# Performance work log

Hardware: AMD Instinct MI355X
Metric: run time of the kernel (lower is better)

## Reference

```python
import jax, jax.numpy as jnp
import numpy as np

# GLOM level-1 geometry (img 256x320, patch 8): feature map 32x40, embd 128
B, C, H, W = 16, 128, 32, 40
GRID = 40          # grid_size = max(256//8, 320//8)
STD = 8.0          # att_stds[0] = int(1/8 * 2**(1+1+4)) with std_scale=4
ATT_TEMP = 1.2     # att_temp_mode 'two', level 1, scale 1.0
EPS = 1e-5


def _norm_cdf(z):
    return 0.5 * (1.0 + jax.scipy.special.erf(z * (1.0 / np.sqrt(2.0))))


def _build_probs():
    # Gaussian-distance neighbor-sampling probabilities, as in GLOM.__init__
    coords = jnp.arange(GRID, dtype=jnp.float32) / STD
    ii, jj = jnp.meshgrid(coords, coords, indexing='ij')          # [G,G]
    pts = jnp.stack([ii.ravel(), jj.ravel()], axis=-1)            # [G*G,2]
    diff = pts[:, None, :] - pts[None, :, :]
    dists = jnp.sqrt(jnp.sum(diff * diff, axis=-1))               # [G*G,G*G]
    p = _norm_cdf(dists + 1.0 / STD) - _norm_cdf(dists)
    p = p * (1.0 - jnp.eye(GRID * GRID, dtype=jnp.float32))       # zero diagonal
    p = jnp.maximum(p, 0.0)
    p = p.reshape(GRID, GRID, GRID, GRID)
    return p[:H, :W, :H, :W]                                      # [H,W,H,W]


def setup_inputs() -> dict:
    key = jax.random.key(0)
    k_x, = jax.random.split(key, 1)
    x = jax.random.normal(k_x, (B, C, H, W), dtype=jnp.float32)
    probs = _build_probs().astype(jnp.float32)
    gamma = jnp.ones((C,), dtype=jnp.float32)
    beta = jnp.zeros((C,), dtype=jnp.float32)
    return {"x": x, "probs": probs, "gamma": gamma, "beta": beta}


def reference(x, probs, gamma, beta):
    # x: [B,C,H,W] level embeddings; probs: [H,W,H,W] distance weights
    b, c, h, w = x.shape
    n = h * w
    xf = x.reshape(b, c, n).transpose(0, 2, 1)                     # [B,N,C]
    # temperature-scaled embedding similarity attention
    logits = jnp.einsum('bnc,bmc->bnm', xf, xf) / (ATT_TEMP * np.sqrt(c))
    att = jax.nn.softmax(logits, axis=-1)                          # [B,N,N]
    # weight by Gaussian-distance neighbor probabilities, renormalize
    wts = att * probs.reshape(n, n)[None]
    wts = wts / (jnp.sum(wts, axis=-1, keepdims=True) + 1e-8)
    agg = jnp.einsum('bnm,bmc->bnc', wts, xf)                      # [B,N,C]
    out = agg.transpose(0, 2, 1).reshape(b, c, h, w)
    # InstanceNorm2d (affine) fused on the attention output
    mu = jnp.mean(out, axis=(2, 3), keepdims=True)
    var = jnp.var(out, axis=(2, 3), keepdims=True)
    out = (out - mu) * jax.lax.rsqrt(var + EPS)
    out = out * gamma[None, :, None, None] + beta[None, :, None, None]
    return out
```

## Files before the change

kernel.cpp:

```cpp
#include <hip/hip_runtime.h>
#include <hip/hip_bf16.h>


#define B_ 16
#define C_ 128
#define N_ 1280
#define BN 80
#define BM 128
#define NT 10
#define LDH 136

typedef __attribute__((ext_vector_type(8))) short short8;
typedef __attribute__((ext_vector_type(4))) float f32x4;
typedef __attribute__((ext_vector_type(4))) unsigned short us4_t;

#define MFMA16(a, bb, c) __builtin_amdgcn_mfma_f32_16x16x32_bf16((a), (bb), (c), 0, 0, 0)

__device__ __forceinline__ unsigned short f2bf(float f) {
    unsigned u = __builtin_bit_cast(unsigned, f);
    u = (u + 0x7FFFu + ((u >> 16) & 1u)) >> 16;
    return (unsigned short)u;
}

__global__ __launch_bounds__(256, 1) void glom_attn_mfma(
    const float* __restrict__ x, const float* __restrict__ probs,
    float* __restrict__ out)
{
    __shared__ __attribute__((aligned(16))) unsigned short AnT[BN][LDH];
    __shared__ __attribute__((aligned(16))) unsigned short XmT[BM][LDH];
    __shared__ __attribute__((aligned(16))) unsigned short Xm [C_][LDH];
    __shared__ __attribute__((aligned(16))) unsigned short Plds[BN][LDH];
    __shared__ float Sred[4][BN], Tred[4][BN], invd_s[BN];

    const int tid = threadIdx.x;
    const int w   = tid >> 6;
    const int l   = tid & 63;
    const int a   = l & 15;
    const int g   = l >> 4;

    const int L  = blockIdx.x;
    const int b  = (L & 7) + 8 * (L >> 7);
    const int nt = (L >> 3) & 15;
    const int n0 = nt * BN;
    const float* Xb = x + (size_t)b * C_ * N_;

    const float INV_SCALE = 0.07365695637359846f;

    #pragma unroll
    for (int k = 0; k < 10; ++k) {
        int f  = tid + 256 * k;
        int c  = f / 20;
        int i4 = f % 20;
        const float4 v = *reinterpret_cast<const float4*>(Xb + c * N_ + n0 + i4 * 4);
        AnT[i4 * 4 + 0][c] = f2bf(v.x);
        AnT[i4 * 4 + 1][c] = f2bf(v.y);
        AnT[i4 * 4 + 2][c] = f2bf(v.z);
        AnT[i4 * 4 + 3][c] = f2bf(v.w);
    }

    f32x4 Y[2][5];
    #pragma unroll
    for (int cl = 0; cl < 2; ++cl)
        #pragma unroll
        for (int nt2 = 0; nt2 < 5; ++nt2)
            #pragma unroll
            for (int rr = 0; rr < 4; ++rr) Y[cl][nt2][rr] = 0.0f;

    float Sp[5][4], Tp[5][4];
    #pragma unroll
    for (int nt2 = 0; nt2 < 5; ++nt2)
        #pragma unroll
        for (int rr = 0; rr < 4; ++rr) { Sp[nt2][rr] = 0.0f; Tp[nt2][rr] = 0.0f; }

    const int cg = tid >> 3, mg = tid & 7;

    for (int mt = 0; mt < NT; ++mt) {
        const int mg0 = mt * BM;
        __syncthreads();

        #pragma unroll
        for (int q = 0; q < 4; ++q) {
            const int mcol = mg0 + 4 * mg + 32 * q;
            const float4 r0 = *reinterpret_cast<const float4*>(Xb + (4*cg+0)*N_ + mcol);
            const float4 r1 = *reinterpret_cast<const float4*>(Xb + (4*cg+1)*N_ + mcol);
            const float4 r2 = *reinterpret_cast<const float4*>(Xb + (4*cg+2)*N_ + mcol);
            const float4 r3 = *reinterpret_cast<const float4*>(Xb + (4*cg+3)*N_ + mcol);
            const int ml = 4 * mg + 32 * q;
            *reinterpret_cast<us4_t*>(&Xm[4*cg+0][ml]) = (us4_t){f2bf(r0.x), f2bf(r0.y), f2bf(r0.z), f2bf(r0.w)};
            *reinterpret_cast<us4_t*>(&Xm[4*cg+1][ml]) = (us4_t){f2bf(r1.x), f2bf(r1.y), f2bf(r1.z), f2bf(r1.w)};
            *reinterpret_cast<us4_t*>(&Xm[4*cg+2][ml]) = (us4_t){f2bf(r2.x), f2bf(r2.y), f2bf(r2.z), f2bf(r2.w)};
            *reinterpret_cast<us4_t*>(&Xm[4*cg+3][ml]) = (us4_t){f2bf(r3.x), f2bf(r3.y), f2bf(r3.z), f2bf(r3.w)};
            *reinterpret_cast<unsigned*>(&XmT[ml+0][4*cg+0]) = (unsigned)f2bf(r0.x) | ((unsigned)f2bf(r1.x) << 16);
            *reinterpret_cast<unsigned*>(&XmT[ml+0][4*cg+2]) = (unsigned)f2bf(r2.x) | ((unsigned)f2bf(r3.x) << 16);
            *reinterpret_cast<unsigned*>(&XmT[ml+1][4*cg+0]) = (unsigned)f2bf(r0.y) | ((unsigned)f2bf(r1.y) << 16);
            *reinterpret_cast<unsigned*>(&XmT[ml+1][4*cg+2]) = (unsigned)f2bf(r2.y) | ((unsigned)f2bf(r3.y) << 16);
            *reinterpret_cast<unsigned*>(&XmT[ml+2][4*cg+0]) = (unsigned)f2bf(r0.z) | ((unsigned)f2bf(r1.z) << 16);
            *reinterpret_cast<unsigned*>(&XmT[ml+2][4*cg+2]) = (unsigned)f2bf(r2.z) | ((unsigned)f2bf(r3.z) << 16);
            *reinterpret_cast<unsigned*>(&XmT[ml+3][4*cg+0]) = (unsigned)f2bf(r0.w) | ((unsigned)f2bf(r1.w) << 16);
            *reinterpret_cast<unsigned*>(&XmT[ml+3][4*cg+2]) = (unsigned)f2bf(r2.w) | ((unsigned)f2bf(r3.w) << 16);
        }
        __syncthreads();

        f32x4 d1[2][5];
        #pragma unroll
        for (int jj = 0; jj < 2; ++jj)
            #pragma unroll
            for (int nt2 = 0; nt2 < 5; ++nt2)
                #pragma unroll
                for (int rr = 0; rr < 4; ++rr) d1[jj][nt2][rr] = 0.0f;

        #pragma unroll
        for (int ks = 0; ks < 4; ++ks) {
            const short8 b0 = *reinterpret_cast<const short8*>(&XmT[32*w      + a][32*ks + 8*g]);
            const short8 b1 = *reinterpret_cast<const short8*>(&XmT[32*w + 16 + a][32*ks + 8*g]);
            #pragma unroll
            for (int nt2 = 0; nt2 < 5; ++nt2) {
                const short8 a1 = *reinterpret_cast<const short8*>(&AnT[16*nt2 + a][32*ks + 8*g]);
                d1[0][nt2] = MFMA16(a1, b0, d1[0][nt2]);
                d1[1][nt2] = MFMA16(a1, b1, d1[1][nt2]);
            }
        }

        #pragma unroll
        for (int jj = 0; jj < 2; ++jj) {
            #pragma unroll
            for (int nt2 = 0; nt2 < 5; ++nt2) {
                const int mcol = mg0 + 32*w + 16*jj + a;
                const size_t pbase = (size_t)(n0 + 16*nt2 + 4*g) * N_ + mcol;
                #pragma unroll
                for (int rr = 0; rr < 4; ++rr) {
                    const float e  = __expf(d1[jj][nt2][rr] * INV_SCALE);
                    const float p  = probs[pbase + (size_t)rr * N_];
                    const float wv = e * p;
                    Sp[nt2][rr] += e;
                    Tp[nt2][rr] += wv;
                    Plds[16*nt2 + 4*g + rr][32*w + 16*jj + a] = f2bf(wv);
                }
            }
        }
        __syncthreads();

        #pragma unroll
        for (int ks2 = 0; ks2 < 4; ++ks2) {
            const short8 a20 = *reinterpret_cast<const short8*>(&Xm[32*w      + a][32*ks2 + 8*g]);
            const short8 a21 = *reinterpret_cast<const short8*>(&Xm[32*w + 16 + a][32*ks2 + 8*g]);
            #pragma unroll
            for (int nt2 = 0; nt2 < 5; ++nt2) {
                const short8 b2 = *reinterpret_cast<const short8*>(&Plds[16*nt2 + a][32*ks2 + 8*g]);
                Y[0][nt2] = MFMA16(a20, b2, Y[0][nt2]);
                Y[1][nt2] = MFMA16(a21, b2, Y[1][nt2]);
            }
        }
    }

    #pragma unroll
    for (int nt2 = 0; nt2 < 5; ++nt2)
        #pragma unroll
        for (int rr = 0; rr < 4; ++rr) {
            #pragma unroll
            for (int d = 1; d < 16; d <<= 1) {
                Sp[nt2][rr] += __shfl_xor(Sp[nt2][rr], d);
                Tp[nt2][rr] += __shfl_xor(Tp[nt2][rr], d);
            }
        }
    if (a == 0) {
        #pragma unroll
        for (int nt2 = 0; nt2 < 5; ++nt2)
            #pragma unroll
            for (int rr = 0; rr < 4; ++rr) {
                Sred[w][16*nt2 + 4*g + rr] = Sp[nt2][rr];
                Tred[w][16*nt2 + 4*g + rr] = Tp[nt2][rr];
            }
    }
    __syncthreads();
    if (tid < BN) {
        const float S = Sred[0][tid] + Sred[1][tid] + Sred[2][tid] + Sred[3][tid];
        const float T = Tred[0][tid] + Tred[1][tid] + Tred[2][tid] + Tred[3][tid];
        invd_s[tid] = 1.0f / (T + 1e-8f * S);
    }
    __syncthreads();

    #pragma unroll
    for (int nt2 = 0; nt2 < 5; ++nt2) {
        const float iv = invd_s[16*nt2 + a];
        #pragma unroll
        for (int cl = 0; cl < 2; ++cl)
            #pragma unroll
            for (int rr = 0; rr < 4; ++rr)
                out[((size_t)b * C_ + 32*w + 16*cl + 4*g + rr) * N_ + n0 + 16*nt2 + a]
                    = Y[cl][nt2][rr] * iv;
    }
}

__global__ __launch_bounds__(256, 4) void glom_inorm_kernel(
    float* __restrict__ out, const float* __restrict__ gamma,
    const float* __restrict__ beta)
{
    const int row = blockIdx.x;
    const int c   = row & (C_ - 1);
    float* p = out + (size_t)row * N_;
    const int t = threadIdx.x;

    float v[5];
    float sm = 0.0f;
    #pragma unroll
    for (int k = 0; k < 5; ++k) { v[k] = p[t + 256 * k]; sm += v[k]; }
    #pragma unroll
    for (int d = 1; d < 64; d <<= 1) sm += __shfl_xor(sm, d);

    __shared__ float red[4];
    const int wid = t >> 6;
    if ((t & 63) == 0) red[wid] = sm;
    __syncthreads();
    const float mu = (red[0] + red[1] + red[2] + red[3]) * (1.0f / (float)N_);

    float sq = 0.0f;
    #pragma unroll
    for (int k = 0; k < 5; ++k) { float d0 = v[k] - mu; sq += d0 * d0; }
    #pragma unroll
    for (int d = 1; d < 64; d <<= 1) sq += __shfl_xor(sq, d);
    __syncthreads();
    if ((t & 63) == 0) red[wid] = sq;
    __syncthreads();
    const float var = (red[0] + red[1] + red[2] + red[3]) * (1.0f / (float)N_);
    const float rs  = rsqrtf(var + 1e-5f);
    const float g   = gamma[c];
    const float be  = beta[c];
    #pragma unroll
    for (int k = 0; k < 5; ++k)
        p[t + 256 * k] = (v[k] - mu) * rs * g + be;
}

extern "C" void kernel_launch(void* const* d_in, const int* in_sizes, int n_in,
                              void* d_out, int out_size, void* d_ws, size_t ws_size,
                              hipStream_t stream)
{
    (void)in_sizes; (void)n_in; (void)out_size; (void)d_ws; (void)ws_size;
    const float* x     = (const float*)d_in[0];
    const float* probs = (const float*)d_in[1];
    const float* gamma = (const float*)d_in[2];
    const float* beta  = (const float*)d_in[3];
    float* out = (float*)d_out;

    glom_attn_mfma<<<dim3(256), dim3(256), 0, stream>>>(x, probs, out);
    glom_inorm_kernel<<<dim3(B_ * C_), dim3(256), 0, stream>>>(out, gamma, beta);
}
```

Measured before the change: 126.4 us.

## Double attention block to 512 threads and prefetch probs before barrier

```diff
diff --git a/kernel.cpp b/kernel.cpp
--- a/kernel.cpp
+++ b/kernel.cpp
@@ -22,7 +22,7 @@
     return (unsigned short)u;
 }
 
-__global__ __launch_bounds__(256, 1) void glom_attn_mfma(
+__global__ __launch_bounds__(512, 1) void glom_attn_mfma(
     const float* __restrict__ x, const float* __restrict__ probs,
     float* __restrict__ out)
 {
@@ -30,7 +30,7 @@
     __shared__ __attribute__((aligned(16))) unsigned short XmT[BM][LDH];
     __shared__ __attribute__((aligned(16))) unsigned short Xm [C_][LDH];
     __shared__ __attribute__((aligned(16))) unsigned short Plds[BN][LDH];
-    __shared__ float Sred[4][BN], Tred[4][BN], invd_s[BN];
+    __shared__ float Sred[8][BN], Tred[8][BN], invd_s[BN];
 
     const int tid = threadIdx.x;
     const int w   = tid >> 6;
@@ -47,8 +47,8 @@
     const float INV_SCALE = 0.07365695637359846f;
 
     #pragma unroll
-    for (int k = 0; k < 10; ++k) {
-        int f  = tid + 256 * k;
+    for (int k = 0; k < 5; ++k) {
+        int f  = tid + 512 * k;
         int c  = f / 20;
         int i4 = f % 20;
         const float4 v = *reinterpret_cast<const float4*>(Xb + c * N_ + n0 + i4 * 4);
@@ -58,13 +58,11 @@
         AnT[i4 * 4 + 3][c] = f2bf(v.w);
     }
 
-    f32x4 Y[2][5];
-    #pragma unroll
-    for (int cl = 0; cl < 2; ++cl)
-        #pragma unroll
-        for (int nt2 = 0; nt2 < 5; ++nt2)
-            #pragma unroll
-            for (int rr = 0; rr < 4; ++rr) Y[cl][nt2][rr] = 0.0f;
+    f32x4 Y[5];
+    #pragma unroll
+    for (int nt2 = 0; nt2 < 5; ++nt2)
+        #pragma unroll
+        for (int rr = 0; rr < 4; ++rr) Y[nt2][rr] = 0.0f;
 
     float Sp[5][4], Tp[5][4];
     #pragma unroll
@@ -72,20 +70,20 @@
         #pragma unroll
         for (int rr = 0; rr < 4; ++rr) { Sp[nt2][rr] = 0.0f; Tp[nt2][rr] = 0.0f; }
 
-    const int cg = tid >> 3, mg = tid & 7;
+    const int cg = tid >> 4, mg = tid & 15;
 
     for (int mt = 0; mt < NT; ++mt) {
         const int mg0 = mt * BM;
         __syncthreads();
 
         #pragma unroll
-        for (int q = 0; q < 4; ++q) {
-            const int mcol = mg0 + 4 * mg + 32 * q;
+        for (int q = 0; q < 2; ++q) {
+            const int mcol = mg0 + 4 * mg + 64 * q;
             const float4 r0 = *reinterpret_cast<const float4*>(Xb + (4*cg+0)*N_ + mcol);
             const float4 r1 = *reinterpret_cast<const float4*>(Xb + (4*cg+1)*N_ + mcol);
             const float4 r2 = *reinterpret_cast<const float4*>(Xb + (4*cg+2)*N_ + mcol);
             const float4 r3 = *reinterpret_cast<const float4*>(Xb + (4*cg+3)*N_ + mcol);
-            const int ml = 4 * mg + 32 * q;
+            const int ml = 4 * mg + 64 * q;
             *reinterpret_cast<us4_t*>(&Xm[4*cg+0][ml]) = (us4_t){f2bf(r0.x), f2bf(r0.y), f2bf(r0.z), f2bf(r0.w)};
             *reinterpret_cast<us4_t*>(&Xm[4*cg+1][ml]) = (us4_t){f2bf(r1.x), f2bf(r1.y), f2bf(r1.z), f2bf(r1.w)};
             *reinterpret_cast<us4_t*>(&Xm[4*cg+2][ml]) = (us4_t){f2bf(r2.x), f2bf(r2.y), f2bf(r2.z), f2bf(r2.w)};
@@ -99,56 +97,53 @@
             *reinterpret_cast<unsigned*>(&XmT[ml+3][4*cg+0]) = (unsigned)f2bf(r0.w) | ((unsigned)f2bf(r1.w) << 16);
             *reinterpret_cast<unsigned*>(&XmT[ml+3][4*cg+2]) = (unsigned)f2bf(r2.w) | ((unsigned)f2bf(r3.w) << 16);
         }
+
+        float pr[5][4];
+        #pragma unroll
+        for (int nt2 = 0; nt2 < 5; ++nt2) {
+            const size_t pbase = (size_t)(n0 + 16*nt2 + 4*g) * N_ + mg0 + 16*w + a;
+            #pragma unroll
+            for (int rr = 0; rr < 4; ++rr)
+                pr[nt2][rr] = probs[pbase + (size_t)rr * N_];
+        }
         __syncthreads();
 
-        f32x4 d1[2][5];
-        #pragma unroll
-        for (int jj = 0; jj < 2; ++jj)
-            #pragma unroll
-            for (int nt2 = 0; nt2 < 5; ++nt2)
-                #pragma unroll
-                for (int rr = 0; rr < 4; ++rr) d1[jj][nt2][rr] = 0.0f;
+        f32x4 d1[5];
+        #pragma unroll
+        for (int nt2 = 0; nt2 < 5; ++nt2)
+            #pragma unroll
+            for (int rr = 0; rr < 4; ++rr) d1[nt2][rr] = 0.0f;
 
         #pragma unroll
         for (int ks = 0; ks < 4; ++ks) {
-            const short8 b0 = *reinterpret_cast<const short8*>(&XmT[32*w      + a][32*ks + 8*g]);
-            const short8 b1 = *reinterpret_cast<const short8*>(&XmT[32*w + 16 + a][32*ks + 8*g]);
+            const short8 b0 = *reinterpret_cast<const short8*>(&XmT[16*w + a][32*ks + 8*g]);
             #pragma unroll
             for (int nt2 = 0; nt2 < 5; ++nt2) {
                 const short8 a1 = *reinterpret_cast<const short8*>(&AnT[16*nt2 + a][32*ks + 8*g]);
-                d1[0][nt2] = MFMA16(a1, b0, d1[0][nt2]);
-                d1[1][nt2] = MFMA16(a1, b1, d1[1][nt2]);
-            }
-        }
-
-        #pragma unroll
-        for (int jj = 0; jj < 2; ++jj) {
-            #pragma unroll
-            for (int nt2 = 0; nt2 < 5; ++nt2) {
-                const int mcol = mg0 + 32*w + 16*jj + a;
-                const size_t pbase = (size_t)(n0 + 16*nt2 + 4*g) * N_ + mcol;
-                #pragma unroll
-                for (int rr = 0; rr < 4; ++rr) {
-                    const float e  = __expf(d1[jj][nt2][rr] * INV_SCALE);
-                    const float p  = probs[pbase + (size_t)rr * N_];
-                    const float wv = e * p;
-                    Sp[nt2][rr] += e;
-                    Tp[nt2][rr] += wv;
-                    Plds[16*nt2 + 4*g + rr][32*w + 16*jj + a] = f2bf(wv);
-                }
+                d1[nt2] = MFMA16(a1, b0, d1[nt2]);
+            }
+        }
+
+        #pragma unroll
+        for (int nt2 = 0; nt2 < 5; ++nt2) {
+            #pragma unroll
+            for (int rr = 0; rr < 4; ++rr) {
+                const float e  = __expf(d1[nt2][rr] * INV_SCALE);
+                const float wv = e * pr[nt2][rr];
+                Sp[nt2][rr] += e;
+                Tp[nt2][rr] += wv;
+                Plds[16*nt2 + 4*g + rr][16*w + a] = f2bf(wv);
             }
         }
         __syncthreads();
 
         #pragma unroll
         for (int ks2 = 0; ks2 < 4; ++ks2) {
-            const short8 a20 = *reinterpret_cast<const short8*>(&Xm[32*w      + a][32*ks2 + 8*g]);
-            const short8 a21 = *reinterpret_cast<const short8*>(&Xm[32*w + 16 + a][32*ks2 + 8*g]);
+            const short8 a2 = *reinterpret_cast<const short8*>(&Xm[16*w + a][32*ks2 + 8*g]);
             #pragma unroll
             for (int nt2 = 0; nt2 < 5; ++nt2) {
                 const short8 b2 = *reinterpret_cast<const short8*>(&Plds[16*nt2 + a][32*ks2 + 8*g]);
-                Y[0][nt2] = MFMA16(a20, b2, Y[0][nt2]);
-                Y[1][nt2] = MFMA16(a21, b2, Y[1][nt2]);
+                Y[nt2] = MFMA16(a2, b2, Y[nt2]);
             }
         }
     }
@@ -174,8 +169,9 @@
     }
     __syncthreads();
     if (tid < BN) {
-        const float S = Sred[0][tid] + Sred[1][tid] + Sred[2][tid] + Sred[3][tid];
-        const float T = Tred[0][tid] + Tred[1][tid] + Tred[2][tid] + Tred[3][tid];
+        float S = 0.0f, T = 0.0f;
+        #pragma unroll
+        for (int ww = 0; ww < 8; ++ww) { S += Sred[ww][tid]; T += Tred[ww][tid]; }
         invd_s[tid] = 1.0f / (T + 1e-8f * S);
     }
     __syncthreads();
@@ -184,11 +180,9 @@
     for (int nt2 = 0; nt2 < 5; ++nt2) {
         const float iv = invd_s[16*nt2 + a];
         #pragma unroll
-        for (int cl = 0; cl < 2; ++cl)
-            #pragma unroll
-            for (int rr = 0; rr < 4; ++rr)
-                out[((size_t)b * C_ + 32*w + 16*cl + 4*g + rr) * N_ + n0 + 16*nt2 + a]
-                    = Y[cl][nt2][rr] * iv;
+        for (int rr = 0; rr < 4; ++rr)
+            out[((size_t)b * C_ + 16*w + 4*g + rr) * N_ + n0 + 16*nt2 + a]
+                = Y[nt2][rr] * iv;
     }
 }
 
@@ -242,6 +236,6 @@
     const float* beta  = (const float*)d_in[3];
     float* out = (float*)d_out;
 
-    glom_attn_mfma<<<dim3(256), dim3(256), 0, stream>>>(x, probs, out);
+    glom_attn_mfma<<<dim3(256), dim3(512), 0, stream>>>(x, probs, out);
     glom_inorm_kernel<<<dim3(B_ * C_), dim3(256), 0, stream>>>(out, gamma, beta);
 }
```

After: 120.6 us. -4.6%, faster.
